# Performance work log

Hardware: AMD Instinct MI355X
Metric: run time of the kernel (lower is better)

The kernel has to match this reference:

```python
import jax, jax.numpy as jnp
import numpy as np

B, N, H, D = 8192, 8, 256, 256          # batch, num_units, hidden_size, input_size
K_ACT = 4                                # k active units
NH_IN, DK_IN, DV_IN = 1, 16, 32          # input attention heads / key / value dims
NH_C, DK_C = 4, 8                        # comm attention heads / key dim
DV_C = H                                 # comm_value_size forced to hidden_size


@jax.custom_vjp
def blocked_grad(x, mask):
    return x

def _bg_fwd(x, mask):
    return x, mask

def _bg_bwd(mask, g):
    return (g * mask, jnp.zeros_like(mask))

blocked_grad.defvjp(_bg_fwd, _bg_bwd)


def setup_inputs() -> dict:
    key = jax.random.key(0)
    ks = jax.random.split(key, 12)
    r = jax.random.normal
    return {
        "x1": r(ks[0], (B, D), jnp.float32),
        "x2": r(ks[1], (B, D), jnp.float32),
        "hs": r(ks[2], (B, N, H), jnp.float32),
        "Wkey": 0.01 * r(ks[3], (D, NH_IN * DK_IN), jnp.float32),
        "bkey": jnp.zeros((NH_IN * DK_IN,), jnp.float32),
        "Wval": 0.01 * r(ks[4], (D, NH_IN * DV_IN), jnp.float32),
        "bval": jnp.zeros((NH_IN * DV_IN,), jnp.float32),
        "Wq": 0.01 * r(ks[5], (N, H, NH_IN * DK_IN), jnp.float32),
        "Wq_": 0.01 * r(ks[6], (N, H, NH_C * DK_C), jnp.float32),
        "Wk_": 0.01 * r(ks[7], (N, H, NH_C * DK_C), jnp.float32),
        "Wv_": 0.01 * r(ks[8], (N, H, NH_C * DV_C), jnp.float32),
        "Wout": 0.01 * r(ks[9], (N, NH_C * DV_C, DV_C), jnp.float32),
        "Wx2h": 0.01 * r(ks[10], (N, DV_IN, 3 * H), jnp.float32),
        "Wh2h": 0.01 * r(ks[11], (N, H, 3 * H), jnp.float32),
    }


def _forward(x1, x2, hs, Wkey, bkey, Wval, bval, Wq, Wq_, Wk_, Wv_, Wout, Wx2h, Wh2h):
    b = x1.shape[0]
    # --- build (B, 3, D): x1, x2 (higher input), null input ---
    null_in = jnp.zeros_like(x1[:, None, :])
    x = jnp.concatenate([x1[:, None, :], x2[:, None, :], null_in], axis=1)  # (B,3,D)

    # --- input attention ---
    kL = (x @ Wkey + bkey).reshape(b, 3, NH_IN, DK_IN).transpose(0, 2, 1, 3)   # (B,h,3,dk)
    vL = (x @ Wval + bval).reshape(b, 3, NH_IN, DV_IN).transpose(0, 2, 1, 3)
    vL = vL.mean(axis=1)                                                        # (B,3,dv)
    qL = jnp.einsum('bnh,nhk->bnk', hs, Wq).reshape(b, N, NH_IN, DK_IN).transpose(0, 2, 1, 3)
    scores = jnp.einsum('bhnd,bhsd->bhns', qL, kL) * (DK_IN ** -0.5)
    scores = scores.mean(axis=1)                                                # (B,N,3)

    # top-k unit selection: deactivate units with largest null-input score
    null_scores = scores[:, :, -1]                                              # (B,N)
    _, idx = jax.lax.top_k(null_scores, N - K_ACT)                              # (B,N-k)
    mask = jnp.ones((b, N), x1.dtype).at[jnp.arange(b)[:, None], idx].set(0.0)

    probs = jax.nn.softmax(scores, axis=-1)                                     # (B,N,3)
    inputs = jnp.einsum('bns,bsd->bnd', probs, vL) * mask[..., None]            # (B,N,dv)

    # --- grouped GRU cell ---
    gate_x = jnp.einsum('bnd,ndo->bno', inputs, Wx2h)                           # (B,N,3H)
    gate_h = jnp.einsum('bnh,nho->bno', hs, Wh2h)
    i_r, i_i, i_n = jnp.split(gate_x, 3, axis=2)
    h_r, h_i, h_n = jnp.split(gate_h, 3, axis=2)
    r = jax.nn.sigmoid(i_r + h_r)
    z = jax.nn.sigmoid(i_i + h_i)
    n = jnp.tanh(i_n + r * h_n)
    hs_new = n + z * (hs - n)                                                   # (B,N,H)

    h_old = hs
    m3 = mask[..., None]                                                        # (B,N,1)
    h_b = blocked_grad(hs_new, m3)

    # --- communication attention across units ---
    q2 = jnp.einsum('bnh,nhk->bnk', h_b, Wq_).reshape(b, N, NH_C, DK_C).transpose(0, 2, 1, 3)
    k2 = jnp.einsum('bnh,nhk->bnk', h_b, Wk_).reshape(b, N, NH_C, DK_C).transpose(0, 2, 1, 3)
    v2 = jnp.einsum('bnh,nhk->bnk', h_b, Wv_).reshape(b, N, NH_C, DV_C).transpose(0, 2, 1, 3)
    att = jnp.einsum('bhnd,bhmd->bhnm', q2, k2) * (DK_C ** -0.5)                # (B,h,N,N)
    att = jax.nn.softmax(att, axis=-1) * mask[:, None, :, None]
    ctx = jnp.einsum('bhnm,bhmd->bhnd', att, v2)                                # (B,h,N,dv)
    ctx = ctx.transpose(0, 2, 1, 3).reshape(b, N, NH_C * DV_C)
    ctx = jnp.einsum('bnd,ndo->bno', ctx, Wout) + h_b                           # (B,N,H)

    return m3 * ctx + (1.0 - m3) * h_old


def reference(x1, x2, hs, Wkey, bkey, Wval, bval, Wq, Wq_, Wk_, Wv_, Wout, Wx2h, Wh2h):
    return _forward(x1, x2, hs, Wkey, bkey, Wval, bval, Wq, Wq_, Wk_, Wv_, Wout, Wx2h, Wh2h)
```

## Files before the change

kernel.cpp:

```cpp
#include <hip/hip_runtime.h>
#include <math.h>


#define B_TOT 8192
#define NU 8
#define HH 256

typedef __attribute__((ext_vector_type(8))) short bf16x8;
typedef __attribute__((ext_vector_type(4))) float f32x4;
typedef unsigned long long u64;

__device__ __forceinline__ float sigm(float x){ return 1.0f/(1.0f+expf(-x)); }

__device__ __forceinline__ unsigned short f2bf(float f){
    union { float f; unsigned int u; } v; v.f = f;
    unsigned int r = v.u + 0x7fffu + ((v.u >> 16) & 1u);
    return (unsigned short)(r >> 16);
}
__device__ __forceinline__ float bf2f(unsigned short h){
    union { unsigned int u; float f; } v; v.u = ((unsigned int)h) << 16;
    return v.f;
}
__device__ __forceinline__ unsigned char f2fp8(float v){
    int p = __builtin_amdgcn_cvt_pk_fp8_f32(v, v, 0, false);
    return (unsigned char)(p & 0xff);
}

#define TG (8*1024*288)
#define TQ (8*1152*256)
#define TO (8*256*1024)
#define TK (48*256)
#define TL (8*16*256)
__global__ void pack_all(const float* __restrict__ Wh2h, const float* __restrict__ Wx2h,
                         const float* __restrict__ Wq_,  const float* __restrict__ Wk_,
                         const float* __restrict__ Wv_,  const float* __restrict__ Wout,
                         const float* __restrict__ Wkey, const float* __restrict__ Wval,
                         const float* __restrict__ Wq,
                         unsigned short* __restrict__ Wg, unsigned short* __restrict__ Wqkv,
                         unsigned char* __restrict__ Wo8, unsigned short* __restrict__ Wkv,
                         unsigned short* __restrict__ Wqt)
{
    long long gidx = (long long)blockIdx.x*256 + threadIdx.x;
    if (gidx < TG) {
        int idx = (int)gidx;
        int k  = idx % 288;
        int pc = (idx / 288) % 1024;
        int n  = idx / (288*1024);
        int cb = pc >> 7, r = pc & 127;
        int g = r >> 5, ol = r & 31;
        int o = cb*32 + ol;
        float v = 0.f;
        if (g == 0)      v = (k < 256) ? Wh2h[((size_t)n*256 + k)*768 + o]
                                       : Wx2h[((size_t)n*32 + (k-256))*768 + o];
        else if (g == 1) v = (k < 256) ? Wh2h[((size_t)n*256 + k)*768 + 256 + o]
                                       : Wx2h[((size_t)n*32 + (k-256))*768 + 256 + o];
        else if (g == 2) v = (k >= 256) ? Wx2h[((size_t)n*32 + (k-256))*768 + 512 + o] : 0.f;
        else             v = (k < 256) ? Wh2h[((size_t)n*256 + k)*768 + 512 + o] : 0.f;
        Wg[idx] = f2bf(v);
        return;
    }
    gidx -= TG;
    if (gidx < TQ) {
        int idx = (int)gidx;
        int k = idx % 256;
        int c = (idx / 256) % 1152;
        int n = idx / (256*1152);
        float v = 0.f;
        if (c < 32)        v = Wq_[((size_t)n*256+k)*32 + c];
        else if (c < 64)   v = Wk_[((size_t)n*256+k)*32 + (c-32)];
        else if (c < 1088) v = Wv_[((size_t)n*256+k)*1024 + (c-64)];
        Wqkv[idx] = f2bf(v);
        return;
    }
    gidx -= TQ;
    if (gidx < TO) {
        int idx = (int)gidx;
        int k = idx % 1024;
        int c = (idx / 1024) % 256;
        int n = idx / (1024*256);
        Wo8[idx] = f2fp8(Wout[((size_t)n*1024 + k)*256 + c]);
        return;
    }
    gidx -= TO;
    if (gidx < TK) {
        int idx = (int)gidx;
        int k = idx & 255, c = idx >> 8;
        float v = (c < 16) ? Wkey[k*16 + c] : Wval[k*32 + (c-16)];
        Wkv[(size_t)c*256 + k] = f2bf(v);
        return;
    }
    gidx -= TK;
    if (gidx < TL) {
        int idx = (int)gidx;
        int k = idx & 255, c = (idx >> 8) & 15, n = idx >> 12;
        Wqt[((size_t)n*16 + c)*256 + k] = f2bf(Wq[((size_t)n*256 + k)*16 + c]);
    }
}

template<int SRC>
__global__ __launch_bounds__(256) void small_gemm(
    const float* __restrict__ A0, const float* __restrict__ A1,
    const unsigned short* __restrict__ Wp, float* __restrict__ C,
    unsigned short* __restrict__ hsb)
{
    constexpr int M    = (SRC == 0) ? 48 : 16;
    constexpr int NJ   = M/16;
    constexpr int AREG = 128*16;
    constexpr int WREG = M*16;
    int row0 = blockIdx.x * 128;
    int n = (SRC == 1) ? blockIdx.y : 0;
    const unsigned short* W = Wp + (size_t)n*M*256;

    __shared__ unsigned short As[2][128*32];
    __shared__ unsigned short Ws[2][M*32];

    int t = threadIdx.x, l = t & 63, w = t >> 6;
    int lr = l & 15, lk = l >> 4;
    int arow = t >> 1, aseg = t & 1;

    f32x4 acc[2][NJ];
    #pragma unroll
    for (int i = 0; i < 2; ++i)
        #pragma unroll
        for (int j = 0; j < NJ; ++j)
            acc[i][j] = (f32x4){0.f,0.f,0.f,0.f};

    bf16x8 au0, au1, wu0, wu1;
    auto loadA = [&](int k0, bf16x8 &u0, bf16x8 &u1) {
        const float* src;
        if (SRC == 0) {
            int gr = row0 + arow;
            src = (gr < B_TOT ? A0 + (size_t)gr*HH : A1 + (size_t)(gr - B_TOT)*HH) + k0 + aseg*16;
        } else {
            src = A0 + (((size_t)(row0 + arow))*NU + n)*HH + k0 + aseg*16;
        }
        const float4* s4 = (const float4*)src;
        float4 f0 = s4[0], f1 = s4[1], f2 = s4[2], f3 = s4[3];
        u0[0]=(short)f2bf(f0.x); u0[1]=(short)f2bf(f0.y); u0[2]=(short)f2bf(f0.z); u0[3]=(short)f2bf(f0.w);
        u0[4]=(short)f2bf(f1.x); u0[5]=(short)f2bf(f1.y); u0[6]=(short)f2bf(f1.z); u0[7]=(short)f2bf(f1.w);
        u1[0]=(short)f2bf(f2.x); u1[1]=(short)f2bf(f2.y); u1[2]=(short)f2bf(f2.z); u1[3]=(short)f2bf(f2.w);
        u1[4]=(short)f2bf(f3.x); u1[5]=(short)f2bf(f3.y); u1[6]=(short)f2bf(f3.z); u1[7]=(short)f2bf(f3.w);
        if (SRC == 1) {
            unsigned short* dp = hsb + ((size_t)n*B_TOT + row0 + arow)*256 + k0 + aseg*16;
            *(bf16x8*)dp       = u0;
            *(bf16x8*)(dp + 8) = u1;
        }
    };
    auto loadW = [&](int k0, bf16x8 &u0, bf16x8 &u1) {
        if (t < M*2) {
            const unsigned short* s = W + (size_t)(t >> 1)*256 + k0 + (t & 1)*16;
            u0 = ((const bf16x8*)s)[0];
            u1 = ((const bf16x8*)s)[1];
        }
    };

    loadA(0, au0, au1);
    loadW(0, wu0, wu1);

    for (int tt = 0; tt < 8; ++tt) {
        char* A_ = (char*)&As[tt & 1][0];
        char* W_ = (char*)&Ws[tt & 1][0];
        *(bf16x8*)(A_ + (aseg*2+0)*AREG + arow*16) = au0;
        *(bf16x8*)(A_ + (aseg*2+1)*AREG + arow*16) = au1;
        if (t < M*2) {
            int wrow = t >> 1, wseg = t & 1;
            *(bf16x8*)(W_ + (wseg*2+0)*WREG + wrow*16) = wu0;
            *(bf16x8*)(W_ + (wseg*2+1)*WREG + wrow*16) = wu1;
        }
        __syncthreads();
        if (tt + 1 < 8) {
            loadA((tt+1)*32, au0, au1);
            loadW((tt+1)*32, wu0, wu1);
        }
        bf16x8 a0 = *(bf16x8*)(A_ + lk*AREG + (w*32 + lr)*16);
        bf16x8 a1 = *(bf16x8*)(A_ + lk*AREG + (w*32 + 16 + lr)*16);
        bf16x8 bq[NJ];
        #pragma unroll
        for (int j = 0; j < NJ; ++j)
            bq[j] = *(bf16x8*)(W_ + lk*WREG + (j*16 + lr)*16);
        #pragma unroll
        for (int j = 0; j < NJ; ++j) {
            acc[0][j] = __builtin_amdgcn_mfma_f32_16x16x32_bf16(a0, bq[j], acc[0][j], 0, 0, 0);
            acc[1][j] = __builtin_amdgcn_mfma_f32_16x16x32_bf16(a1, bq[j], acc[1][j], 0, 0, 0);
        }
    }

    float* Cb = (SRC == 0) ? C : C + (size_t)n*B_TOT*16;
    #pragma unroll
    for (int i = 0; i < 2; ++i)
        #pragma unroll
        for (int j = 0; j < NJ; ++j)
            #pragma unroll
            for (int reg = 0; reg < 4; ++reg) {
                int r = row0 + w*32 + i*16 + lk*4 + reg;
                Cb[(size_t)r*M + j*16 + lr] = acc[i][j][reg];
            }
}

__global__ __launch_bounds__(256) void score_mask_inputs(
    const float* __restrict__ KV,
    const float* __restrict__ qL,
    const float* __restrict__ bkey, const float* __restrict__ bval,
    unsigned short* __restrict__ inputs, float* __restrict__ maskf)
{
    int t  = threadIdx.x;
    int gb = blockIdx.x*32 + (t >> 3);
    int n  = t & 7, l = t & 63;

    float q[16];
    const float* qp = qL + ((size_t)n*B_TOT + gb)*16;
    #pragma unroll
    for (int i = 0; i < 4; ++i) *(float4*)&q[i*4] = ((const float4*)qp)[i];

    const float* kv0 = KV + (size_t)gb*48;
    const float* kv1 = KV + (size_t)(B_TOT + gb)*48;

    float s0 = 0.f, s1 = 0.f, sn = 0.f;
    #pragma unroll
    for (int k = 0; k < 16; ++k) {
        float bk = bkey[k];
        s0 += q[k]*(kv0[k] + bk);
        s1 += q[k]*(kv1[k] + bk);
        sn += q[k]*bk;
    }
    s0 *= 0.25f; s1 *= 0.25f; sn *= 0.25f;

    float mx = fmaxf(s0, fmaxf(s1, sn));
    float e0 = expf(s0-mx), e1 = expf(s1-mx), en = expf(sn-mx);
    float inv = 1.f/(e0+e1+en);
    float p0 = e0*inv, p1 = e1*inv, pn = en*inv;

    int rank = 0;
    #pragma unroll
    for (int m = 0; m < 8; ++m) {
        float sm = __shfl(sn, (l & ~7) + m, 64);
        if (sm > sn || (sm == sn && m < n)) rank++;
    }
    float mk = (rank < 4) ? 0.f : 1.f;
    maskf[(size_t)gb*8 + n] = mk;

    unsigned short* op = inputs + ((size_t)n*B_TOT + gb)*32;
    #pragma unroll
    for (int db = 0; db < 4; ++db) {
        bf16x8 o;
        #pragma unroll
        for (int e = 0; e < 8; ++e) {
            int d = db*8 + e;
            float bv = bval[d];
            float v = mk*(p0*(kv0[16+d]+bv) + p1*(kv1[16+d]+bv) + pn*bv);
            o[e] = (short)f2bf(v);
        }
        *(bf16x8*)&op[db*8] = o;
    }
}

__global__ __launch_bounds__(256) void attn_kernel(
    const unsigned short* __restrict__ QKb,
    const unsigned char*  __restrict__ V2,
    unsigned char* __restrict__ CTX,
    const float* __restrict__ maskf, int Bc, int c0)
{
    int wid = threadIdx.x >> 6;
    int l   = threadIdx.x & 63;
    int b   = blockIdx.x*4 + wid;
    int gb  = c0 + b;

    __shared__ float qk[4][8][64];
    __shared__ float P[4][4][8][8];

    for (int it = 0; it < 8; ++it) {
        int idx = l + 64*it;
        int n = idx >> 6, c = idx & 63;
        qk[wid][n][c] = bf2f(QKb[((size_t)n*Bc + b)*64 + c]);
    }
    __syncthreads();

    for (int it = 0; it < 4; ++it) {
        int idx = l + 64*it;
        int h = idx >> 6, n = (idx >> 3) & 7, m = idx & 7;
        float s = 0.f;
        #pragma unroll
        for (int dk = 0; dk < 8; ++dk) s += qk[wid][n][h*8 + dk]*qk[wid][m][32 + h*8 + dk];
        P[wid][h][n][m] = s * 0.35355339059327373f;
    }
    __syncthreads();

    if (l < 32) {
        int h = l >> 3, n = l & 7;
        float mx = -1e30f;
        for (int m = 0; m < 8; ++m) mx = fmaxf(mx, P[wid][h][n][m]);
        float e[8], sum = 0.f;
        for (int m = 0; m < 8; ++m) { e[m] = expf(P[wid][h][n][m]-mx); sum += e[m]; }
        float scl = maskf[(size_t)gb*8 + n] / sum;
        for (int m = 0; m < 8; ++m) P[wid][h][n][m] = e[m]*scl;
    }
    __syncthreads();

    #pragma unroll
    for (int it = 0; it < 2; ++it) {
        int colb = (l + 64*it)*8;
        int h = colb >> 8;
        float acc[8][8];
        #pragma unroll
        for (int n = 0; n < 8; ++n)
            #pragma unroll
            for (int c = 0; c < 8; ++c) acc[n][c] = 0.f;
        for (int m = 0; m < 8; ++m) {
            uint2 v8 = *(const uint2*)&V2[((size_t)m*Bc + b)*1024 + colb];
            float vf[8];
            vf[0] = __builtin_amdgcn_cvt_f32_fp8(v8.x, 0);
            vf[1] = __builtin_amdgcn_cvt_f32_fp8(v8.x, 1);
            vf[2] = __builtin_amdgcn_cvt_f32_fp8(v8.x, 2);
            vf[3] = __builtin_amdgcn_cvt_f32_fp8(v8.x, 3);
            vf[4] = __builtin_amdgcn_cvt_f32_fp8(v8.y, 0);
            vf[5] = __builtin_amdgcn_cvt_f32_fp8(v8.y, 1);
            vf[6] = __builtin_amdgcn_cvt_f32_fp8(v8.y, 2);
            vf[7] = __builtin_amdgcn_cvt_f32_fp8(v8.y, 3);
            #pragma unroll
            for (int n = 0; n < 8; ++n) {
                float p = P[wid][h][n][m];
                #pragma unroll
                for (int c = 0; c < 8; ++c) acc[n][c] += p*vf[c];
            }
        }
        #pragma unroll
        for (int n = 0; n < 8; ++n) {
            int lo = __builtin_amdgcn_cvt_pk_fp8_f32(acc[n][0], acc[n][1], 0,  false);
            lo     = __builtin_amdgcn_cvt_pk_fp8_f32(acc[n][2], acc[n][3], lo, true);
            int hi = __builtin_amdgcn_cvt_pk_fp8_f32(acc[n][4], acc[n][5], 0,  false);
            hi     = __builtin_amdgcn_cvt_pk_fp8_f32(acc[n][6], acc[n][7], hi, true);
            uint2 o; o.x = (unsigned int)lo; o.y = (unsigned int)hi;
            *(uint2*)&CTX[((size_t)n*Bc + b)*1024 + colb] = o;
        }
    }
}

template<int MODE, int TN>
__global__ __launch_bounds__(512) void gemm_mfma(
    const unsigned short* __restrict__ hsb,
    const unsigned short* __restrict__ inputs,
    const unsigned short* __restrict__ Asrc,
    const unsigned short* __restrict__ Wp,
    unsigned short* __restrict__ hsnb,
    unsigned short* __restrict__ QKb,
    unsigned char*  __restrict__ V2,
    int Bc, int c0)
{
    constexpr int KW   = (MODE==0) ? 288 : 256;
    constexpr int M    = (MODE==0) ? 1024 : 1152;
    constexpr int BM   = 256;
    constexpr int NJ   = TN/16;
    constexpr int NT   = KW/32;
    constexpr int CB   = M/TN;
    constexpr int AREG = BM*16;
    constexpr int WREG = TN*16;

    int bid = blockIdx.x;
    int n   = bid & 7;
    int loc = bid >> 3;
    int col0 = (loc % CB) * TN;
    int row0 = (loc / CB) * BM;

    __shared__ unsigned short As[2][BM*32];
    __shared__ unsigned short Ws[2][TN*32];

    int t = threadIdx.x;
    int l = t & 63, w = t >> 6;
    int lr = l & 15, lk = l >> 4;

    int arow = t >> 1, aseg = t & 1;
    int wrow = t & 127, wslot = t >> 7;

    f32x4 acc[2][NJ];
    #pragma unroll
    for (int i = 0; i < 2; ++i)
        #pragma unroll
        for (int j = 0; j < NJ; ++j)
            acc[i][j] = (f32x4){0.f,0.f,0.f,0.f};

    bf16x8 aA0, aA1, wA0;
    bf16x8 aB0, aB1, wB0;

    auto loadA = [&](int k0, bf16x8 &u0, bf16x8 &u1) {
        const unsigned short* s;
        if (MODE == 0) {
            if (k0 < 256) s = hsb + ((size_t)n*B_TOT + c0 + row0 + arow)*256 + k0 + aseg*16;
            else          s = inputs + ((size_t)n*B_TOT + c0 + row0 + arow)*32 + aseg*16;
        } else {
            s = Asrc + ((size_t)n*Bc + row0 + arow)*256 + k0 + aseg*16;
        }
        u0 = ((const bf16x8*)s)[0];
        u1 = ((const bf16x8*)s)[1];
    };
    auto loadW = [&](int k0, bf16x8 &u0) {
        const unsigned short* s = Wp + ((size_t)n*M + col0 + wrow)*(size_t)KW + k0 + wslot*8;
        u0 = *(const bf16x8*)s;
    };
    auto stage = [&](char* A_, char* W_, bf16x8 a0, bf16x8 a1, bf16x8 w0) {
        *(bf16x8*)(A_ + (aseg*2+0)*AREG + arow*16) = a0;
        *(bf16x8*)(A_ + (aseg*2+1)*AREG + arow*16) = a1;
        *(bf16x8*)(W_ + wslot*WREG + wrow*16) = w0;
    };
    auto compute = [&](char* A_, char* W_) {
        bf16x8 a0 = *(bf16x8*)(A_ + lk*AREG + (w*32 + lr)*16);
        bf16x8 a1 = *(bf16x8*)(A_ + lk*AREG + (w*32 + 16 + lr)*16);
        #pragma unroll
        for (int j = 0; j < NJ; ++j) {
            bf16x8 b = *(bf16x8*)(W_ + lk*WREG + (j*16 + lr)*16);
            acc[0][j] = __builtin_amdgcn_mfma_f32_16x16x32_bf16(a0, b, acc[0][j], 0, 0, 0);
            acc[1][j] = __builtin_amdgcn_mfma_f32_16x16x32_bf16(a1, b, acc[1][j], 0, 0, 0);
        }
    };

    char* AE = (char*)&As[0][0]; char* AO = (char*)&As[1][0];
    char* WE = (char*)&Ws[0][0]; char* WO = (char*)&Ws[1][0];

    loadA(0,  aA0, aA1);  loadW(0,  wA0);
    loadA(32, aB0, aB1);  loadW(32, wB0);

    int tt = 0;
    for (; tt + 1 < NT; tt += 2) {
        stage(AE, WE, aA0, aA1, wA0);
        __syncthreads();
        if (tt + 2 < NT) { loadA((tt+2)*32, aA0, aA1); loadW((tt+2)*32, wA0); }
        compute(AE, WE);

        stage(AO, WO, aB0, aB1, wB0);
        __syncthreads();
        if (tt + 3 < NT) { loadA((tt+3)*32, aB0, aB1); loadW((tt+3)*32, wB0); }
        compute(AO, WO);
    }
    if (tt < NT) {
        stage(AE, WE, aA0, aA1, wA0);
        __syncthreads();
        compute(AE, WE);
    }

    if constexpr (MODE == 0) {
        #pragma unroll
        for (int i = 0; i < 2; ++i) {
            int rbase = row0 + w*32 + i*16 + lk*4;
            #pragma unroll
            for (int half = 0; half < 2; ++half) {
                int o = (col0 >> 2) + half*16 + lr;
                #pragma unroll
                for (int reg = 0; reg < 4; ++reg) {
                    int r = rbase + reg;
                    float rs = acc[i][0+half][reg];
                    float zs = acc[i][2+half][reg];
                    float gx = acc[i][4+half][reg];
                    float gh = acc[i][6+half][reg];
                    float hold = bf2f(hsb[((size_t)n*B_TOT + c0 + r)*256 + o]);
                    float rr = sigm(rs), z = sigm(zs);
                    float nn = tanhf(gx + rr*gh);
                    float h  = nn + z*(hold - nn);
                    hsnb[((size_t)n*Bc + r)*256 + o] = f2bf(h);
                }
            }
        }
    } else {
        #pragma unroll
        for (int i = 0; i < 2; ++i) {
            #pragma unroll
            for (int j = 0; j < NJ; ++j) {
                int c = col0 + j*16 + lr;
                #pragma unroll
                for (int reg = 0; reg < 4; ++reg) {
                    int r = row0 + w*32 + i*16 + lk*4 + reg;
                    float v = acc[i][j][reg];
                    if (c < 64) QKb[((size_t)n*Bc + r)*64 + c] = f2bf(v);
                    else        V2 [((size_t)n*Bc + r)*1024 + (c-64)] = f2fp8(v);
                }
            }
        }
    }
}

__global__ __launch_bounds__(512) void gemm_out_fp8(
    const unsigned char* __restrict__ CTX,
    const unsigned char* __restrict__ Wo8,
    const unsigned short* __restrict__ hsnb,
    const float* __restrict__ hs_glob,
    const float* __restrict__ maskf,
    float* __restrict__ outp,
    int Bc, int c0)
{
    constexpr int BM = 256, TN = 128, NJ = 8, NT = 32, CB = 2;
    constexpr int AREG = BM*8;
    constexpr int WREG = TN*8;

    int bid = blockIdx.x;
    int n   = bid & 7;
    int loc = bid >> 3;
    int col0 = (loc % CB) * TN;
    int row0 = (loc / CB) * BM;

    __shared__ unsigned char As[2][BM*32];
    __shared__ unsigned char Ws[2][TN*32];

    int t = threadIdx.x;
    int l = t & 63, w = t >> 6;
    int lr = l & 15, lk = l >> 4;
    int arow = t >> 1, ahalf = t & 1;
    int wrow = t & 127, wslot = t >> 7;

    f32x4 acc[2][NJ];
    #pragma unroll
    for (int i = 0; i < 2; ++i)
        #pragma unroll
        for (int j = 0; j < NJ; ++j)
            acc[i][j] = (f32x4){0.f,0.f,0.f,0.f};

    u64 aA0, aA1, wA0;
    u64 aB0, aB1, wB0;

    auto loadA = [&](int k0, u64 &u0, u64 &u1) {
        const unsigned char* s = CTX + ((size_t)n*Bc + row0 + arow)*1024 + k0 + ahalf*16;
        u0 = *(const u64*)s;
        u1 = *(const u64*)(s + 8);
    };
    auto loadW = [&](int k0, u64 &u0) {
        const unsigned char* s = Wo8 + ((size_t)n*256 + col0 + wrow)*1024 + k0 + wslot*8;
        u0 = *(const u64*)s;
    };
    auto stage = [&](unsigned char* A_, unsigned char* W_, u64 a0, u64 a1, u64 w0) {
        *(u64*)(A_ + (ahalf*2+0)*AREG + arow*8) = a0;
        *(u64*)(A_ + (ahalf*2+1)*AREG + arow*8) = a1;
        *(u64*)(W_ + wslot*WREG + wrow*8) = w0;
    };
    auto compute = [&](unsigned char* A_, unsigned char* W_) {
        long a0 = *(const long*)(A_ + lk*AREG + (w*32 + lr)*8);
        long a1 = *(const long*)(A_ + lk*AREG + (w*32 + 16 + lr)*8);
        #pragma unroll
        for (int j = 0; j < NJ; ++j) {
            long b = *(const long*)(W_ + lk*WREG + (j*16 + lr)*8);
            acc[0][j] = __builtin_amdgcn_mfma_f32_16x16x32_fp8_fp8(a0, b, acc[0][j], 0, 0, 0);
            acc[1][j] = __builtin_amdgcn_mfma_f32_16x16x32_fp8_fp8(a1, b, acc[1][j], 0, 0, 0);
        }
    };

    unsigned char* AE = &As[0][0]; unsigned char* AO = &As[1][0];
    unsigned char* WE = &Ws[0][0]; unsigned char* WO = &Ws[1][0];

    loadA(0,  aA0, aA1);  loadW(0,  wA0);
    loadA(32, aB0, aB1);  loadW(32, wB0);

    for (int tt = 0; tt < NT; tt += 2) {
        stage(AE, WE, aA0, aA1, wA0);
        __syncthreads();
        if (tt + 2 < NT) { loadA((tt+2)*32, aA0, aA1); loadW((tt+2)*32, wA0); }
        compute(AE, WE);

        stage(AO, WO, aB0, aB1, wB0);
        __syncthreads();
        if (tt + 3 < NT) { loadA((tt+3)*32, aB0, aB1); loadW((tt+3)*32, wB0); }
        compute(AO, WO);
    }

    #pragma unroll
    for (int i = 0; i < 2; ++i) {
        #pragma unroll
        for (int reg = 0; reg < 4; ++reg) {
            int r = row0 + w*32 + i*16 + lk*4 + reg;
            float mkv = maskf[(size_t)(c0 + r)*8 + n];
            size_t gi0 = (((size_t)(c0 + r))*NU + n)*HH;
            #pragma unroll
            for (int j = 0; j < NJ; ++j) {
                int c = col0 + j*16 + lr;
                float v;
                if (mkv != 0.f) v = acc[i][j][reg] + bf2f(hsnb[((size_t)n*Bc + r)*256 + c]);
                else            v = hs_glob[gi0 + c];
                outp[gi0 + c] = v;
            }
        }
    }
}

extern "C" void kernel_launch(void* const* d_in, const int* in_sizes, int n_in,
                              void* d_out, int out_size, void* d_ws, size_t ws_size,
                              hipStream_t stream)
{
    const float* x1   = (const float*)d_in[0];
    const float* x2   = (const float*)d_in[1];
    const float* hs   = (const float*)d_in[2];
    const float* Wkey = (const float*)d_in[3];
    const float* bkey = (const float*)d_in[4];
    const float* Wval = (const float*)d_in[5];
    const float* bval = (const float*)d_in[6];
    const float* Wq   = (const float*)d_in[7];
    const float* Wq_  = (const float*)d_in[8];
    const float* Wk_  = (const float*)d_in[9];
    const float* Wv_  = (const float*)d_in[10];
    const float* Wout = (const float*)d_in[11];
    const float* Wx2h = (const float*)d_in[12];
    const float* Wh2h = (const float*)d_in[13];
    float* out = (float*)d_out;

    char* ws = (char*)d_ws;
    size_t off = 0;
    auto alloc = [&](size_t bytes) -> void* {
        void* p = (void*)(ws + off);
        off = (off + bytes + 255) & ~(size_t)255;
        return p;
    };
    unsigned short* Wg     = (unsigned short*)alloc((size_t)8*1024*288*2);
    unsigned short* Wqkv   = (unsigned short*)alloc((size_t)8*1152*256*2);
    unsigned char*  Wo8    = (unsigned char*) alloc((size_t)8*256*1024);
    unsigned short* Wkv    = (unsigned short*)alloc((size_t)48*256*2);
    unsigned short* Wqt    = (unsigned short*)alloc((size_t)8*16*256*2);
    unsigned short* inputs = (unsigned short*)alloc((size_t)8*B_TOT*32*2);
    float*          maskf  = (float*)         alloc((size_t)B_TOT*8*4);
    float*          KV     = (float*)         alloc((size_t)2*B_TOT*48*4);
    float*          qL     = (float*)         alloc((size_t)8*B_TOT*16*4);
    unsigned short* hsb    = (unsigned short*)alloc((size_t)8*B_TOT*256*2);
    size_t persist = off;

    const size_t perB = 8*256*2 + 8*64*2 + 8*1024 + 8*1024;
    int Bc = B_TOT;
    while (Bc > 256 && persist + (size_t)Bc*perB + 65536 > ws_size) Bc >>= 1;
    unsigned short* hsnb = (unsigned short*)alloc((size_t)8*Bc*256*2);
    unsigned short* QKb  = (unsigned short*)alloc((size_t)8*Bc*64*2);
    unsigned char*  V2   = (unsigned char*) alloc((size_t)8*Bc*1024);
    unsigned char*  CTX  = (unsigned char*) alloc((size_t)8*Bc*1024);

    const long long packN = (long long)TG + TQ + TO + TK + TL;
    pack_all<<<(int)((packN + 255)/256), 256, 0, stream>>>(
        Wh2h, Wx2h, Wq_, Wk_, Wv_, Wout, Wkey, Wval, Wq,
        Wg, Wqkv, Wo8, Wkv, Wqt);

    small_gemm<0><<<dim3(2*B_TOT/128), 256, 0, stream>>>(x1, x2, Wkv, KV, nullptr);
    small_gemm<1><<<dim3(B_TOT/128, 8), 256, 0, stream>>>(hs, nullptr, Wqt, qL, hsb);
    score_mask_inputs<<<B_TOT/32, 256, 0, stream>>>(KV, qL, bkey, bval, inputs, maskf);

    for (int c0 = 0; c0 < B_TOT; c0 += Bc) {
        int RB = Bc / 256;
        gemm_mfma<0,128><<<dim3(RB*8*8), 512, 0, stream>>>(
            hsb, inputs, nullptr, Wg, hsnb, nullptr, nullptr, Bc, c0);
        gemm_mfma<1,128><<<dim3(RB*9*8), 512, 0, stream>>>(
            hsb, nullptr, hsnb, Wqkv, nullptr, QKb, V2, Bc, c0);
        attn_kernel<<<Bc/4, 256, 0, stream>>>(QKb, V2, CTX, maskf, Bc, c0);
        gemm_out_fp8<<<dim3(RB*2*8), 512, 0, stream>>>(
            CTX, Wo8, hsnb, hs, maskf, out, Bc, c0);
    }
}
```

Measured before the change: 304.0 us.

## Compute full 256-column output tile per block in fp8 output GEMM

The output projection GEMM now uses 1024-thread blocks that each cover all 256 output columns for a 256-row tile. Warps are arranged 4x4, each computing a 64x64 sub-tile, which replaces the earlier split into two 128-column blocks that both reloaded the same CTX rows. The aim is to halve global reads of the A operand and improve MFMA operand reuse per LDS load. The cost is half as many blocks, larger LDS and more registers per thread, which may reduce occupancy and parallelism.

```diff
diff --git a/kernel.cpp b/kernel.cpp
--- a/kernel.cpp
+++ b/kernel.cpp
@@ -476,7 +476,7 @@
     }
 }
 
-__global__ __launch_bounds__(512) void gemm_out_fp8(
+__global__ __launch_bounds__(1024) void gemm_out_fp8(
     const unsigned char* __restrict__ CTX,
     const unsigned char* __restrict__ Wo8,
     const unsigned short* __restrict__ hsnb,
@@ -485,88 +485,84 @@
     float* __restrict__ outp,
     int Bc, int c0)
 {
-    constexpr int BM = 256, TN = 128, NJ = 8, NT = 32, CB = 2;
+    constexpr int BM = 256, NT = 32;
     constexpr int AREG = BM*8;
-    constexpr int WREG = TN*8;
+    constexpr int WREG = 256*8;
 
     int bid = blockIdx.x;
     int n   = bid & 7;
-    int loc = bid >> 3;
-    int col0 = (loc % CB) * TN;
-    int row0 = (loc / CB) * BM;
+    int row0 = (bid >> 3) * BM;
 
     __shared__ unsigned char As[2][BM*32];
-    __shared__ unsigned char Ws[2][TN*32];
+    __shared__ unsigned char Ws[2][256*32];
 
     int t = threadIdx.x;
     int l = t & 63, w = t >> 6;
+    int wr = w >> 2, wc = w & 3;
     int lr = l & 15, lk = l >> 4;
-    int arow = t >> 1, ahalf = t & 1;
-    int wrow = t & 127, wslot = t >> 7;
-
-    f32x4 acc[2][NJ];
-    #pragma unroll
-    for (int i = 0; i < 2; ++i)
-        #pragma unroll
-        for (int j = 0; j < NJ; ++j)
+    int arow = t >> 2, aslot = t & 3;
+
+    f32x4 acc[4][4];
+    #pragma unroll
+    for (int i = 0; i < 4; ++i)
+        #pragma unroll
+        for (int j = 0; j < 4; ++j)
             acc[i][j] = (f32x4){0.f,0.f,0.f,0.f};
 
-    u64 aA0, aA1, wA0;
-    u64 aB0, aB1, wB0;
-
-    auto loadA = [&](int k0, u64 &u0, u64 &u1) {
-        const unsigned char* s = CTX + ((size_t)n*Bc + row0 + arow)*1024 + k0 + ahalf*16;
-        u0 = *(const u64*)s;
-        u1 = *(const u64*)(s + 8);
+    u64 aA0, wA0, aB0, wB0;
+
+    auto loadA = [&](int k0, u64 &u0) {
+        u0 = *(const u64*)(CTX + ((size_t)n*Bc + row0 + arow)*1024 + k0 + aslot*8);
     };
     auto loadW = [&](int k0, u64 &u0) {
-        const unsigned char* s = Wo8 + ((size_t)n*256 + col0 + wrow)*1024 + k0 + wslot*8;
-        u0 = *(const u64*)s;
-    };
-    auto stage = [&](unsigned char* A_, unsigned char* W_, u64 a0, u64 a1, u64 w0) {
-        *(u64*)(A_ + (ahalf*2+0)*AREG + arow*8) = a0;
-        *(u64*)(A_ + (ahalf*2+1)*AREG + arow*8) = a1;
-        *(u64*)(W_ + wslot*WREG + wrow*8) = w0;
+        u0 = *(const u64*)(Wo8 + ((size_t)n*256 + arow)*1024 + k0 + aslot*8);
+    };
+    auto stage = [&](unsigned char* A_, unsigned char* W_, u64 a0, u64 w0) {
+        *(u64*)(A_ + aslot*AREG + arow*8) = a0;
+        *(u64*)(W_ + aslot*WREG + arow*8) = w0;
     };
     auto compute = [&](unsigned char* A_, unsigned char* W_) {
-        long a0 = *(const long*)(A_ + lk*AREG + (w*32 + lr)*8);
-        long a1 = *(const long*)(A_ + lk*AREG + (w*32 + 16 + lr)*8);
-        #pragma unroll
-        for (int j = 0; j < NJ; ++j) {
-            long b = *(const long*)(W_ + lk*WREG + (j*16 + lr)*8);
-            acc[0][j] = __builtin_amdgcn_mfma_f32_16x16x32_fp8_fp8(a0, b, acc[0][j], 0, 0, 0);
-            acc[1][j] = __builtin_amdgcn_mfma_f32_16x16x32_fp8_fp8(a1, b, acc[1][j], 0, 0, 0);
+        long a[4];
+        #pragma unroll
+        for (int i = 0; i < 4; ++i)
+            a[i] = *(const long*)(A_ + lk*AREG + (wr*64 + i*16 + lr)*8);
+        #pragma unroll
+        for (int j = 0; j < 4; ++j) {
+            long b = *(const long*)(W_ + lk*WREG + (wc*64 + j*16 + lr)*8);
+            #pragma unroll
+            for (int i = 0; i < 4; ++i)
+                acc[i][j] = __builtin_amdgcn_mfma_f32_16x16x32_fp8_fp8(a[i], b, acc[i][j], 0, 0, 0);
         }
     };
 
     unsigned char* AE = &As[0][0]; unsigned char* AO = &As[1][0];
     unsigned char* WE = &Ws[0][0]; unsigned char* WO = &Ws[1][0];
 
-    loadA(0,  aA0, aA1);  loadW(0,  wA0);
-    loadA(32, aB0, aB1);  loadW(32, wB0);
+    loadA(0,  aA0);  loadW(0,  wA0);
+    loadA(32, aB0);  loadW(32, wB0);
 
     for (int tt = 0; tt < NT; tt += 2) {
-        stage(AE, WE, aA0, aA1, wA0);
+        stage(AE, WE, aA0, wA0);
         __syncthreads();
-        if (tt + 2 < NT) { loadA((tt+2)*32, aA0, aA1); loadW((tt+2)*32, wA0); }
+        if (tt + 2 < NT) { loadA((tt+2)*32, aA0); loadW((tt+2)*32, wA0); }
         compute(AE, WE);
 
-        stage(AO, WO, aB0, aB1, wB0);
+        stage(AO, WO, aB0, wB0);
         __syncthreads();
-        if (tt + 3 < NT) { loadA((tt+3)*32, aB0, aB1); loadW((tt+3)*32, wB0); }
+        if (tt + 3 < NT) { loadA((tt+3)*32, aB0); loadW((tt+3)*32, wB0); }
         compute(AO, WO);
     }
 
     #pragma unroll
-    for (int i = 0; i < 2; ++i) {
+    for (int i = 0; i < 4; ++i) {
         #pragma unroll
         for (int reg = 0; reg < 4; ++reg) {
-            int r = row0 + w*32 + i*16 + lk*4 + reg;
+            int r = row0 + wr*64 + i*16 + lk*4 + reg;
             float mkv = maskf[(size_t)(c0 + r)*8 + n];
             size_t gi0 = (((size_t)(c0 + r))*NU + n)*HH;
             #pragma unroll
-            for (int j = 0; j < NJ; ++j) {
-                int c = col0 + j*16 + lr;
+            for (int j = 0; j < 4; ++j) {
+                int c = wc*64 + j*16 + lr;
                 float v;
                 if (mkv != 0.f) v = acc[i][j][reg] + bf2f(hsnb[((size_t)n*Bc + r)*256 + c]);
                 else            v = hs_glob[gi0 + c];
@@ -639,7 +635,7 @@
         gemm_mfma<1,128><<<dim3(RB*9*8), 512, 0, stream>>>(
             hsb, nullptr, hsnb, Wqkv, nullptr, QKb, V2, Bc, c0);
         attn_kernel<<<Bc/4, 256, 0, stream>>>(QKb, V2, CTX, maskf, Bc, c0);
-        gemm_out_fp8<<<dim3(RB*2*8), 512, 0, stream>>>(
+        gemm_out_fp8<<<dim3(RB*8), 1024, 0, stream>>>(
             CTX, Wo8, hsnb, hs, maskf, out, Bc, c0);
     }
 }
```

New measurement: 308.1 us. No clear change (+1.4%).
